# Kernel optimization log

Hardware: AMD Instinct MI355X
Metric: run time of the kernel (lower is better)

Reference implementation:

```python
import jax, jax.numpy as jnp
import numpy as np

B, T, C, H = 2, 2048, 1024, 16
HD = C // H  # head dim = 64


def setup_inputs() -> dict:
    key = jax.random.key(0)
    k1, k2, k3 = jax.random.split(key, 3)
    scale = 0.02
    x = jax.random.normal(k1, (B, T, C), dtype=jnp.float32)
    w_attn = jax.random.normal(k2, (C, 3 * C), dtype=jnp.float32) * scale
    b_attn = jnp.zeros((3 * C,), dtype=jnp.float32)
    w_proj = jax.random.normal(k3, (C, C), dtype=jnp.float32) * scale
    b_proj = jnp.zeros((C,), dtype=jnp.float32)
    return {"x": x, "w_attn": w_attn, "b_attn": b_attn, "w_proj": w_proj, "b_proj": b_proj}


def reference(x, w_attn, b_attn, w_proj, b_proj):
    b, t, c = x.shape
    qkv = x @ w_attn + b_attn  # [B,T,3C]
    q, k, v = jnp.split(qkv, 3, axis=-1)
    # [B,T,C] -> [B,H,T,HD]
    q = q.reshape(b, t, H, HD).transpose(0, 2, 1, 3)
    k = k.reshape(b, t, H, HD).transpose(0, 2, 1, 3)
    v = v.reshape(b, t, H, HD).transpose(0, 2, 1, 3)
    att = jnp.einsum('bhqd,bhkd->bhqk', q, k) * (1.0 / jnp.sqrt(jnp.float32(HD)))
    causal = jnp.tril(jnp.ones((t, t), dtype=bool))  # [T,T]
    att = jnp.where(causal[None, None, :, :], att, jnp.float32(-jnp.inf))
    att = jax.nn.softmax(att, axis=-1)
    y = jnp.einsum('bhqk,bhkd->bhqd', att, v)
    y = y.transpose(0, 2, 1, 3).reshape(b, t, c)
    return y @ w_proj + b_proj
```

## Files before the change

kernel.cpp:

```cpp
#include <hip/hip_runtime.h>


typedef unsigned short u16;
typedef unsigned short u16x8 __attribute__((ext_vector_type(8)));
typedef __bf16 bf16x8 __attribute__((ext_vector_type(8)));
typedef __bf16 bf16x4 __attribute__((ext_vector_type(4)));
typedef float f32x4 __attribute__((ext_vector_type(4)));

#define MFMA16(a, b, c) __builtin_amdgcn_mfma_f32_16x16x32_bf16(a, b, c, 0, 0, 0)

static __device__ __forceinline__ u16 f2b(float f) {
  union { float f; unsigned int i; } x; x.f = f;
  unsigned int r = x.i + 0x7fffu + ((x.i >> 16) & 1u);
  return (u16)(r >> 16);
}
static __device__ __forceinline__ float b2f(u16 u) {
  union { unsigned int i; float f; } x; x.i = ((unsigned int)u) << 16; return x.f;
}

static __device__ __forceinline__ void gload_lds16(const u16* g, u16* l) {
#if defined(__HIP_DEVICE_COMPILE__)
  __builtin_amdgcn_global_load_lds(
      (const __attribute__((address_space(1))) unsigned int*)g,
      (__attribute__((address_space(3))) unsigned int*)l,
      16, 0, 0);
#else
  (void)g; (void)l;
#endif
}

__global__ __launch_bounds__(256) void cast_f32_bf16(
    const float* __restrict__ in, u16* __restrict__ out) {
  int i = (blockIdx.x * 256 + threadIdx.x) * 8;
  float4 a = *(const float4*)&in[i];
  float4 b = *(const float4*)&in[i + 4];
  u16x8 o;
  o[0] = f2b(a.x); o[1] = f2b(a.y); o[2] = f2b(a.z); o[3] = f2b(a.w);
  o[4] = f2b(b.x); o[5] = f2b(b.y); o[6] = f2b(b.z); o[7] = f2b(b.w);
  *(u16x8*)&out[i] = o;
}

__global__ __launch_bounds__(256) void transpose_f32_bf16(
    const float* __restrict__ in, u16* __restrict__ out, int R, int Cc) {
  __shared__ u16 tile[32][33];
  int bx = blockIdx.x, by = blockIdx.y;
  int tx = threadIdx.x, ty = threadIdx.y;
#pragma unroll
  for (int i = 0; i < 4; i++) {
    int r = by * 32 + ty + i * 8;
    int c = bx * 32 + tx;
    tile[ty + i * 8][tx] = f2b(in[r * Cc + c]);
  }
  __syncthreads();
#pragma unroll
  for (int i = 0; i < 4; i++) {
    int r = bx * 32 + ty + i * 8;
    int c = by * 32 + tx;
    out[r * R + c] = tile[tx][ty + i * 8];
  }
}

__global__ __launch_bounds__(256) void transpose_v(
    const u16* __restrict__ in, u16* __restrict__ out) {
  int bh = blockIdx.y;
  int t = blockIdx.x * 128 + (threadIdx.x & 127);
  int dg = (threadIdx.x >> 7) * 32;
  const u16* src = in + (bh * 2048 + t) * 64;
  u16* dst = out + bh * 64 * 2048 + t;
#pragma unroll
  for (int i = 0; i < 32; i++) {
    int d = dg + i;
    dst[d * 2048] = src[d];
  }
}

template <int MODE>
__global__ __launch_bounds__(256, 2) void gemm_bt(
    const u16* __restrict__ A, const u16* __restrict__ Bt,
    const float* __restrict__ bias, float* __restrict__ out,
    u16* __restrict__ Qb, u16* __restrict__ Kb, u16* __restrict__ Vb,
    int M, int N, int K) {
  __shared__ u16 lA[128 * 32];
  __shared__ u16 lB[128 * 32];

  const int tid = threadIdx.x;
  const int lane = tid & 63;
  const int w = tid >> 6;
  const int wm = (w >> 1) * 64, wn = (w & 1) * 64;
  const int l15 = lane & 15, quad = lane >> 4;
  const int m0 = blockIdx.y * 128, n0 = blockIdx.x * 128;

  const int srow = lane >> 2;
  const int scol = (lane & 3) * 8;

  f32x4 acc[4][4] = {};

  for (int k0 = 0; k0 < K; k0 += 32) {
    __syncthreads();
#pragma unroll
    for (int h = 0; h < 2; h++) {
      int r = h * 64 + w * 16 + srow;
      gload_lds16(&A[(m0 + r) * K + k0 + scol], &lA[h * 2048 + w * 512 + lane * 8]);
      gload_lds16(&Bt[(n0 + r) * K + k0 + scol], &lB[h * 2048 + w * 512 + lane * 8]);
    }
    __syncthreads();

    bf16x8 af[4], bfr[4];
#pragma unroll
    for (int mi = 0; mi < 4; mi++)
      af[mi] = *(const bf16x8*)&lA[(wm + mi * 16 + l15) * 32 + quad * 8];
#pragma unroll
    for (int ni = 0; ni < 4; ni++)
      bfr[ni] = *(const bf16x8*)&lB[(wn + ni * 16 + l15) * 32 + quad * 8];
#pragma unroll
    for (int mi = 0; mi < 4; mi++)
#pragma unroll
      for (int ni = 0; ni < 4; ni++)
        acc[mi][ni] = MFMA16(af[mi], bfr[ni], acc[mi][ni]);
  }

#pragma unroll
  for (int mi = 0; mi < 4; mi++) {
#pragma unroll
    for (int ni = 0; ni < 4; ni++) {
      int n = n0 + wn + ni * 16 + l15;
      float bv = bias[n];
#pragma unroll
      for (int reg = 0; reg < 4; reg++) {
        int m = m0 + wm + mi * 16 + quad * 4 + reg;
        float v = acc[mi][ni][reg] + bv;
        if (MODE == 1) {
          out[m * N + n] = v;
        } else {
          int which = n >> 10;
          if (which == 1) v *= 0.18033688011112042f;
          int hn = n & 1023;
          int hh = hn >> 6, d = hn & 63;
          int b = m >> 11, t = m & 2047;
          u16* dst = (which == 0) ? Qb : ((which == 1) ? Kb : Vb);
          dst[(((b << 4) + hh) * 2048 + t) * 64 + d] = f2b(v);
        }
      }
    }
  }
}

__global__ __launch_bounds__(256, 4) void attn_split(
    const u16* __restrict__ Qg, const u16* __restrict__ Kg,
    const u16* __restrict__ Vt, u16* __restrict__ Yg,
    u16* __restrict__ Opart, float* __restrict__ lpart) {
  __shared__ u16 lk[64 * 72];
  __shared__ u16 lvt[64 * 72];

  const int x = blockIdx.x;
  const int bh = blockIdx.y;
  int qt, s, ns;
  if (x < 8)       { qt = x;                s = 0;            ns = 1; }
  else if (x < 24) { int r = x - 8;  qt = 8  + (r >> 1); s = r & 1; ns = 2; }
  else if (x < 48) { int r = x - 24; qt = 16 + r / 3;    s = r % 3; ns = 3; }
  else             { int r = x - 48; qt = 24 + (r >> 2); s = r & 3; ns = 4; }
  const int kts = s * 8;
  const int kend = (kts + 8 < qt + 1) ? (kts + 8) : (qt + 1);

  const int tid = threadIdx.x;
  const int lane = tid & 63;
  const int w = tid >> 6;
  const int l15 = lane & 15, quad = lane >> 4;
  const int qbase = qt * 64;
  const int base = bh * 2048 * 64;
  const int vbase = bh * 64 * 2048;

  const int sr = tid >> 3;
  const int sc = (tid & 7) * 8;

  const u16* qrow = Qg + base + (qbase + w * 16 + l15) * 64;
  bf16x8 bq0 = *(const bf16x8*)&qrow[quad * 8];
  bf16x8 bq1 = *(const bf16x8*)&qrow[32 + quad * 8];

  u16x8 onesu = {0x3F80, 0x3F80, 0x3F80, 0x3F80, 0x3F80, 0x3F80, 0x3F80, 0x3F80};
  bf16x8 ones = *(const bf16x8*)&onesu;

  const u16* kp = Kg + base;
  const u16* vp = Vt + vbase;

  u16x8 kr[2], vr[2];
  {
    int kvb = kts * 64;
#pragma unroll
    for (int h = 0; h < 2; h++) {
      int r = sr + h * 32;
      kr[h] = *(const u16x8*)&kp[(kvb + r) * 64 + sc];
      vr[h] = *(const u16x8*)&vp[r * 2048 + kvb + sc];
    }
  }

  f32x4 oacc[4] = {};
  f32x4 lacc = {};

  for (int kt = kts; kt < kend; kt++) {
    __syncthreads();
#pragma unroll
    for (int h = 0; h < 2; h++) {
      int r = sr + h * 32;
      *(u16x8*)&lk[r * 72 + sc] = kr[h];
      *(u16x8*)&lvt[r * 72 + sc] = vr[h];
    }
    __syncthreads();
    if (kt + 1 < kend) {
      int kvb = (kt + 1) * 64;
#pragma unroll
      for (int h = 0; h < 2; h++) {
        int r = sr + h * 32;
        kr[h] = *(const u16x8*)&kp[(kvb + r) * 64 + sc];
        vr[h] = *(const u16x8*)&vp[r * 2048 + kvb + sc];
      }
    }

    const bool diag = (kt == qt);
    const int qloc = w * 16 + l15;

#pragma unroll
    for (int u = 0; u < 2; u++) {
      bf16x8 pa;
#pragma unroll
      for (int half = 0; half < 2; half++) {
        int nt = 2 * u + half;
        bf16x8 ak0 = *(const bf16x8*)&lk[(nt * 16 + l15) * 72 + quad * 8];
        bf16x8 ak1 = *(const bf16x8*)&lk[(nt * 16 + l15) * 72 + 32 + quad * 8];
        f32x4 st = {};
        st = MFMA16(ak0, bq0, st);
        st = MFMA16(ak1, bq1, st);
#pragma unroll
        for (int reg = 0; reg < 4; reg++) {
          float sv = st[reg];
          if (diag && (nt * 16 + quad * 4 + reg) > qloc) sv = -1e30f;
          pa[half * 4 + reg] = (__bf16)exp2f(sv);
        }
      }
      lacc = MFMA16(pa, ones, lacc);
#pragma unroll
      for (int dt = 0; dt < 4; dt++) {
        const u16* vrow = &lvt[(dt * 16 + l15) * 72 + u * 32 + quad * 4];
        bf16x4 lo = *(const bf16x4*)&vrow[0];
        bf16x4 hi = *(const bf16x4*)&vrow[16];
        bf16x8 bv;
#pragma unroll
        for (int j = 0; j < 4; j++) { bv[j] = lo[j]; bv[4 + j] = hi[j]; }
        oacc[dt] = MFMA16(pa, bv, oacc[dt]);
      }
    }
  }

  if (ns == 1) {
    const int b = bh >> 4, hh = bh & 15;
    float inv[4];
#pragma unroll
    for (int reg = 0; reg < 4; reg++) inv[reg] = 1.0f / lacc[reg];
#pragma unroll
    for (int dt = 0; dt < 4; dt++)
#pragma unroll
      for (int reg = 0; reg < 4; reg++) {
        int q = qbase + w * 16 + quad * 4 + reg;
        int col = hh * 64 + dt * 16 + l15;
        Yg[(b * 2048 + q) * 1024 + col] = f2b(oacc[dt][reg] * inv[reg]);
      }
  } else {
    const int p = bh * 80 + x;
    u16* op = Opart + p * 4096 + (w * 16) * 64;
#pragma unroll
    for (int dt = 0; dt < 4; dt++)
#pragma unroll
      for (int reg = 0; reg < 4; reg++)
        op[(quad * 4 + reg) * 64 + dt * 16 + l15] = f2b(oacc[dt][reg]);
    if (l15 == 0) {
#pragma unroll
      for (int reg = 0; reg < 4; reg++)
        lpart[p * 64 + w * 16 + quad * 4 + reg] = lacc[reg];
    }
  }
}

__global__ __launch_bounds__(256) void attn_combine(
    const u16* __restrict__ Opart, const float* __restrict__ lpart,
    u16* __restrict__ Yg) {
  const int qt = 8 + blockIdx.x;
  const int bh = blockIdx.y;
  const int tid = threadIdx.x;
  const int row = tid >> 2;
  const int cg = (tid & 3) * 16;
  int xb, ns;
  if (qt < 16)      { xb = 8  + (qt - 8) * 2;  ns = 2; }
  else if (qt < 24) { xb = 24 + (qt - 16) * 3; ns = 3; }
  else              { xb = 48 + (qt - 24) * 4; ns = 4; }

  float acc[16] = {};
  float lsum = 0.f;
  for (int i = 0; i < ns; i++) {
    int p = bh * 80 + xb + i;
    lsum += lpart[p * 64 + row];
    const u16* oprow = Opart + p * 4096 + row * 64 + cg;
    u16x8 a = *(const u16x8*)&oprow[0];
    u16x8 b = *(const u16x8*)&oprow[8];
#pragma unroll
    for (int j = 0; j < 8; j++) { acc[j] += b2f(a[j]); acc[8 + j] += b2f(b[j]); }
  }
  float inv = 1.0f / lsum;
  u16x8 o0, o1;
#pragma unroll
  for (int j = 0; j < 8; j++) { o0[j] = f2b(acc[j] * inv); o1[j] = f2b(acc[8 + j] * inv); }
  const int b = bh >> 4, hh = bh & 15;
  u16* y = Yg + ((long)(b * 2048 + qt * 64 + row)) * 1024 + hh * 64 + cg;
  *(u16x8*)&y[0] = o0;
  *(u16x8*)&y[8] = o1;
}

__global__ __launch_bounds__(256, 4) void attn_kernel(
    const u16* __restrict__ Qg, const u16* __restrict__ Kg,
    const u16* __restrict__ Vt, u16* __restrict__ Yg) {
  __shared__ u16 lk[64 * 72];
  __shared__ u16 lvt[64 * 72];

  const int qt = 31 - blockIdx.x;
  const int bh = blockIdx.y;
  const int tid = threadIdx.x;
  const int lane = tid & 63;
  const int w = tid >> 6;
  const int l15 = lane & 15, quad = lane >> 4;
  const int qbase = qt * 64;
  const int base = bh * 2048 * 64;
  const int vbase = bh * 64 * 2048;
  const int sr = tid >> 3;
  const int sc = (tid & 7) * 8;

  const u16* qrow = Qg + base + (qbase + w * 16 + l15) * 64;
  bf16x8 bq0 = *(const bf16x8*)&qrow[quad * 8];
  bf16x8 bq1 = *(const bf16x8*)&qrow[32 + quad * 8];

  u16x8 onesu = {0x3F80, 0x3F80, 0x3F80, 0x3F80, 0x3F80, 0x3F80, 0x3F80, 0x3F80};
  bf16x8 ones = *(const bf16x8*)&onesu;

  const u16* kp = Kg + base;
  const u16* vp = Vt + vbase;

  u16x8 kr[2], vr[2];
#pragma unroll
  for (int h = 0; h < 2; h++) {
    int r = sr + h * 32;
    kr[h] = *(const u16x8*)&kp[r * 64 + sc];
    vr[h] = *(const u16x8*)&vp[r * 2048 + sc];
  }

  f32x4 oacc[4] = {};
  f32x4 lacc = {};

  for (int kt = 0; kt <= qt; kt++) {
    __syncthreads();
#pragma unroll
    for (int h = 0; h < 2; h++) {
      int r = sr + h * 32;
      *(u16x8*)&lk[r * 72 + sc] = kr[h];
      *(u16x8*)&lvt[r * 72 + sc] = vr[h];
    }
    __syncthreads();
    if (kt < qt) {
      int kvb = (kt + 1) * 64;
#pragma unroll
      for (int h = 0; h < 2; h++) {
        int r = sr + h * 32;
        kr[h] = *(const u16x8*)&kp[(kvb + r) * 64 + sc];
        vr[h] = *(const u16x8*)&vp[r * 2048 + kvb + sc];
      }
    }

    const bool diag = (kt == qt);
    const int qloc = w * 16 + l15;
#pragma unroll
    for (int u = 0; u < 2; u++) {
      bf16x8 pa;
#pragma unroll
      for (int half = 0; half < 2; half++) {
        int nt = 2 * u + half;
        bf16x8 ak0 = *(const bf16x8*)&lk[(nt * 16 + l15) * 72 + quad * 8];
        bf16x8 ak1 = *(const bf16x8*)&lk[(nt * 16 + l15) * 72 + 32 + quad * 8];
        f32x4 st = {};
        st = MFMA16(ak0, bq0, st);
        st = MFMA16(ak1, bq1, st);
#pragma unroll
        for (int reg = 0; reg < 4; reg++) {
          float sv = st[reg];
          if (diag && (nt * 16 + quad * 4 + reg) > qloc) sv = -1e30f;
          pa[half * 4 + reg] = (__bf16)exp2f(sv);
        }
      }
      lacc = MFMA16(pa, ones, lacc);
#pragma unroll
      for (int dt = 0; dt < 4; dt++) {
        const u16* vrow = &lvt[(dt * 16 + l15) * 72 + u * 32 + quad * 4];
        bf16x4 lo = *(const bf16x4*)&vrow[0];
        bf16x4 hi = *(const bf16x4*)&vrow[16];
        bf16x8 bv;
#pragma unroll
        for (int j = 0; j < 4; j++) { bv[j] = lo[j]; bv[4 + j] = hi[j]; }
        oacc[dt] = MFMA16(pa, bv, oacc[dt]);
      }
    }
  }

  const int b = bh >> 4, hh = bh & 15;
  float inv[4];
#pragma unroll
  for (int reg = 0; reg < 4; reg++) inv[reg] = 1.0f / lacc[reg];
#pragma unroll
  for (int dt = 0; dt < 4; dt++)
#pragma unroll
    for (int reg = 0; reg < 4; reg++) {
      int q = qbase + w * 16 + quad * 4 + reg;
      int col = hh * 64 + dt * 16 + l15;
      Yg[(b * 2048 + q) * 1024 + col] = f2b(oacc[dt][reg] * inv[reg]);
    }
}

extern "C" void kernel_launch(void* const* d_in, const int* in_sizes, int n_in,
                              void* d_out, int out_size, void* d_ws, size_t ws_size,
                              hipStream_t stream) {
  const float* x      = (const float*)d_in[0];
  const float* w_attn = (const float*)d_in[1];
  const float* b_attn = (const float*)d_in[2];
  const float* w_proj = (const float*)d_in[3];
  const float* b_proj = (const float*)d_in[4];
  float* out = (float*)d_out;

  char* ws = (char*)d_ws;
  u16* wattnT = (u16*)(ws);
  u16* wprojT = (u16*)(ws + 6291456);
  u16* xb     = (u16*)(ws + 8388608);
  u16* Vt     = xb;
  u16* Qb     = (u16*)(ws + 16777216);
  u16* Kb     = (u16*)(ws + 25165824);
  u16* Vb     = (u16*)(ws + 33554432);
  u16* Yb     = (u16*)(ws + 41943040);
  u16* Opart  = (u16*)(ws + 50331648);
  float* lpart = (float*)(ws + 71303168);

  const bool split = (ws_size >= 71958528ULL);

  cast_f32_bf16<<<2048, 256, 0, stream>>>(x, xb);
  transpose_f32_bf16<<<dim3(96, 32), dim3(32, 8), 0, stream>>>(w_attn, wattnT, 1024, 3072);
  transpose_f32_bf16<<<dim3(32, 32), dim3(32, 8), 0, stream>>>(w_proj, wprojT, 1024, 1024);
  gemm_bt<0><<<dim3(24, 32), 256, 0, stream>>>(xb, wattnT, b_attn, nullptr,
                                               Qb, Kb, Vb, 4096, 3072, 1024);
  transpose_v<<<dim3(16, 32), 256, 0, stream>>>(Vb, Vt);
  if (split) {
    attn_split<<<dim3(80, 32), 256, 0, stream>>>(Qb, Kb, Vt, Yb, Opart, lpart);
    attn_combine<<<dim3(24, 32), 256, 0, stream>>>(Opart, lpart, Yb);
  } else {
    attn_kernel<<<dim3(32, 32), 256, 0, stream>>>(Qb, Kb, Vt, Yb);
  }
  gemm_bt<1><<<dim3(8, 32), 256, 0, stream>>>(Yb, wprojT, b_proj, out,
                                              nullptr, nullptr, nullptr, 4096, 1024, 1024);
}
```

Before: 200.3 us.

## Process two query tiles per attention block to reuse K/V tiles

Each split-attention block now handles a pair of adjacent 64-row query tiles (128 rows), computing two score/probability streams against each loaded K/V tile. This halves the K/V global loads and LDS staging per query row and halves the grid size. The blocks are also launched in reverse order so the heaviest work starts first. In exchange, register pressure rises from doubling the accumulators, and there are fewer, larger blocks, which may lower occupancy. The combine kernel and the partial buffer layout are adjusted to match.

```diff
diff --git a/kernel.cpp b/kernel.cpp
--- a/kernel.cpp
+++ b/kernel.cpp
@@ -152,30 +152,36 @@
   __shared__ u16 lk[64 * 72];
   __shared__ u16 lvt[64 * 72];
 
-  const int x = blockIdx.x;
+  const int x = 39 - blockIdx.x;
   const int bh = blockIdx.y;
-  int qt, s, ns;
-  if (x < 8)       { qt = x;                s = 0;            ns = 1; }
-  else if (x < 24) { int r = x - 8;  qt = 8  + (r >> 1); s = r & 1; ns = 2; }
-  else if (x < 48) { int r = x - 24; qt = 16 + r / 3;    s = r % 3; ns = 3; }
-  else             { int r = x - 48; qt = 24 + (r >> 2); s = r & 3; ns = 4; }
+  int p, s, ns;
+  if (x < 4)       { p = x;          s = 0;           ns = 1; }
+  else if (x < 12) { int r = x - 4;  p = 4 + (r >> 1);  s = r & 1;  ns = 2; }
+  else if (x < 24) { int r = x - 12; p = 8 + r / 3;     s = r % 3;  ns = 3; }
+  else             { int r = x - 24; p = 12 + (r >> 2); s = r & 3;  ns = 4; }
   const int kts = s * 8;
-  const int kend = (kts + 8 < qt + 1) ? (kts + 8) : (qt + 1);
+  const int ktotal = 2 * p + 2;
+  const int kend = (kts + 8 < ktotal) ? (kts + 8) : ktotal;
+  const int qtA = 2 * p;
 
   const int tid = threadIdx.x;
   const int lane = tid & 63;
   const int w = tid >> 6;
   const int l15 = lane & 15, quad = lane >> 4;
-  const int qbase = qt * 64;
   const int base = bh * 2048 * 64;
   const int vbase = bh * 64 * 2048;
 
   const int sr = tid >> 3;
   const int sc = (tid & 7) * 8;
 
-  const u16* qrow = Qg + base + (qbase + w * 16 + l15) * 64;
-  bf16x8 bq0 = *(const bf16x8*)&qrow[quad * 8];
-  bf16x8 bq1 = *(const bf16x8*)&qrow[32 + quad * 8];
+  const u16* qrA = Qg + base + (qtA * 64 + w * 16 + l15) * 64;
+  bf16x8 bq0A = *(const bf16x8*)&qrA[quad * 8];
+  bf16x8 bq1A = *(const bf16x8*)&qrA[32 + quad * 8];
+  const u16* qrB = qrA + 64 * 64;
+  bf16x8 bq0B = *(const bf16x8*)&qrB[quad * 8];
+  bf16x8 bq1B = *(const bf16x8*)&qrB[32 + quad * 8];
+
+  const int qgA = qtA * 64 + w * 16 + l15;
 
   u16x8 onesu = {0x3F80, 0x3F80, 0x3F80, 0x3F80, 0x3F80, 0x3F80, 0x3F80, 0x3F80};
   bf16x8 ones = *(const bf16x8*)&onesu;
@@ -194,8 +200,8 @@
     }
   }
 
-  f32x4 oacc[4] = {};
-  f32x4 lacc = {};
+  f32x4 oA[4] = {}, oB[4] = {};
+  f32x4 lA4 = {}, lB4 = {};
 
   for (int kt = kts; kt < kend; kt++) {
     __syncthreads();
@@ -216,28 +222,37 @@
       }
     }
 
-    const bool diag = (kt == qt);
-    const int qloc = w * 16 + l15;
+    const bool mA = (kt >= qtA);
+    const bool mB = (kt == qtA + 1);
 
 #pragma unroll
     for (int u = 0; u < 2; u++) {
-      bf16x8 pa;
+      bf16x8 paA, paB;
 #pragma unroll
       for (int half = 0; half < 2; half++) {
         int nt = 2 * u + half;
         bf16x8 ak0 = *(const bf16x8*)&lk[(nt * 16 + l15) * 72 + quad * 8];
         bf16x8 ak1 = *(const bf16x8*)&lk[(nt * 16 + l15) * 72 + 32 + quad * 8];
-        f32x4 st = {};
-        st = MFMA16(ak0, bq0, st);
-        st = MFMA16(ak1, bq1, st);
+        f32x4 stA = {};
+        stA = MFMA16(ak0, bq0A, stA);
+        stA = MFMA16(ak1, bq1A, stA);
+        f32x4 stB = {};
+        stB = MFMA16(ak0, bq0B, stB);
+        stB = MFMA16(ak1, bq1B, stB);
+        int kv0 = kt * 64 + nt * 16 + quad * 4;
 #pragma unroll
         for (int reg = 0; reg < 4; reg++) {
-          float sv = st[reg];
-          if (diag && (nt * 16 + quad * 4 + reg) > qloc) sv = -1e30f;
-          pa[half * 4 + reg] = (__bf16)exp2f(sv);
+          int kv = kv0 + reg;
+          float svA = stA[reg];
+          if (mA && kv > qgA) svA = -1e30f;
+          float svB = stB[reg];
+          if (mB && kv > qgA + 64) svB = -1e30f;
+          paA[half * 4 + reg] = (__bf16)exp2f(svA);
+          paB[half * 4 + reg] = (__bf16)exp2f(svB);
         }
       }
-      lacc = MFMA16(pa, ones, lacc);
+      lA4 = MFMA16(paA, ones, lA4);
+      lB4 = MFMA16(paB, ones, lB4);
 #pragma unroll
       for (int dt = 0; dt < 4; dt++) {
         const u16* vrow = &lvt[(dt * 16 + l15) * 72 + u * 32 + quad * 4];
@@ -246,36 +261,47 @@
         bf16x8 bv;
 #pragma unroll
         for (int j = 0; j < 4; j++) { bv[j] = lo[j]; bv[4 + j] = hi[j]; }
-        oacc[dt] = MFMA16(pa, bv, oacc[dt]);
+        oA[dt] = MFMA16(paA, bv, oA[dt]);
+        oB[dt] = MFMA16(paB, bv, oB[dt]);
       }
     }
   }
 
   if (ns == 1) {
     const int b = bh >> 4, hh = bh & 15;
-    float inv[4];
-#pragma unroll
-    for (int reg = 0; reg < 4; reg++) inv[reg] = 1.0f / lacc[reg];
+    float invA[4], invB[4];
+#pragma unroll
+    for (int reg = 0; reg < 4; reg++) {
+      invA[reg] = 1.0f / lA4[reg];
+      invB[reg] = 1.0f / lB4[reg];
+    }
 #pragma unroll
     for (int dt = 0; dt < 4; dt++)
 #pragma unroll
       for (int reg = 0; reg < 4; reg++) {
-        int q = qbase + w * 16 + quad * 4 + reg;
+        int qA = qtA * 64 + w * 16 + quad * 4 + reg;
         int col = hh * 64 + dt * 16 + l15;
-        Yg[(b * 2048 + q) * 1024 + col] = f2b(oacc[dt][reg] * inv[reg]);
+        Yg[(b * 2048 + qA) * 1024 + col] = f2b(oA[dt][reg] * invA[reg]);
+        Yg[(b * 2048 + qA + 64) * 1024 + col] = f2b(oB[dt][reg] * invB[reg]);
       }
   } else {
-    const int p = bh * 80 + x;
-    u16* op = Opart + p * 4096 + (w * 16) * 64;
+    const int pidx = bh * 40 + x;
+    u16* op = Opart + pidx * 8192;
 #pragma unroll
     for (int dt = 0; dt < 4; dt++)
 #pragma unroll
-      for (int reg = 0; reg < 4; reg++)
-        op[(quad * 4 + reg) * 64 + dt * 16 + l15] = f2b(oacc[dt][reg]);
+      for (int reg = 0; reg < 4; reg++) {
+        int rA = w * 16 + quad * 4 + reg;
+        op[rA * 64 + dt * 16 + l15] = f2b(oA[dt][reg]);
+        op[(rA + 64) * 64 + dt * 16 + l15] = f2b(oB[dt][reg]);
+      }
     if (l15 == 0) {
 #pragma unroll
-      for (int reg = 0; reg < 4; reg++)
-        lpart[p * 64 + w * 16 + quad * 4 + reg] = lacc[reg];
+      for (int reg = 0; reg < 4; reg++) {
+        int rA = w * 16 + quad * 4 + reg;
+        lpart[pidx * 128 + rA] = lA4[reg];
+        lpart[pidx * 128 + rA + 64] = lB4[reg];
+      }
     }
   }
 }
@@ -283,35 +309,39 @@
 __global__ __launch_bounds__(256) void attn_combine(
     const u16* __restrict__ Opart, const float* __restrict__ lpart,
     u16* __restrict__ Yg) {
-  const int qt = 8 + blockIdx.x;
+  const int pp = 4 + blockIdx.x;
   const int bh = blockIdx.y;
   const int tid = threadIdx.x;
-  const int row = tid >> 2;
-  const int cg = (tid & 3) * 16;
+  const int row = tid >> 1;
+  const int cg = (tid & 1) * 32;
   int xb, ns;
-  if (qt < 16)      { xb = 8  + (qt - 8) * 2;  ns = 2; }
-  else if (qt < 24) { xb = 24 + (qt - 16) * 3; ns = 3; }
-  else              { xb = 48 + (qt - 24) * 4; ns = 4; }
-
-  float acc[16] = {};
+  if (pp < 8)       { xb = 4  + (pp - 4) * 2;  ns = 2; }
+  else if (pp < 12) { xb = 12 + (pp - 8) * 3;  ns = 3; }
+  else              { xb = 24 + (pp - 12) * 4; ns = 4; }
+
+  float acc[32] = {};
   float lsum = 0.f;
   for (int i = 0; i < ns; i++) {
-    int p = bh * 80 + xb + i;
-    lsum += lpart[p * 64 + row];
-    const u16* oprow = Opart + p * 4096 + row * 64 + cg;
-    u16x8 a = *(const u16x8*)&oprow[0];
-    u16x8 b = *(const u16x8*)&oprow[8];
-#pragma unroll
-    for (int j = 0; j < 8; j++) { acc[j] += b2f(a[j]); acc[8 + j] += b2f(b[j]); }
+    int pidx = bh * 40 + xb + i;
+    lsum += lpart[pidx * 128 + row];
+    const u16* oprow = Opart + pidx * 8192 + row * 64 + cg;
+#pragma unroll
+    for (int v = 0; v < 4; v++) {
+      u16x8 a = *(const u16x8*)&oprow[v * 8];
+#pragma unroll
+      for (int j = 0; j < 8; j++) acc[v * 8 + j] += b2f(a[j]);
+    }
   }
   float inv = 1.0f / lsum;
-  u16x8 o0, o1;
-#pragma unroll
-  for (int j = 0; j < 8; j++) { o0[j] = f2b(acc[j] * inv); o1[j] = f2b(acc[8 + j] * inv); }
   const int b = bh >> 4, hh = bh & 15;
-  u16* y = Yg + ((long)(b * 2048 + qt * 64 + row)) * 1024 + hh * 64 + cg;
-  *(u16x8*)&y[0] = o0;
-  *(u16x8*)&y[8] = o1;
+  u16* y = Yg + ((long)(b * 2048 + pp * 128 + row)) * 1024 + hh * 64 + cg;
+#pragma unroll
+  for (int v = 0; v < 4; v++) {
+    u16x8 o;
+#pragma unroll
+    for (int j = 0; j < 8; j++) o[j] = f2b(acc[v * 8 + j] * inv);
+    *(u16x8*)&y[v * 8] = o;
+  }
 }
 
 __global__ __launch_bounds__(256, 4) void attn_kernel(
@@ -451,8 +481,8 @@
                                                Qb, Kb, Vb, 4096, 3072, 1024);
   transpose_v<<<dim3(16, 32), 256, 0, stream>>>(Vb, Vt);
   if (split) {
-    attn_split<<<dim3(80, 32), 256, 0, stream>>>(Qb, Kb, Vt, Yb, Opart, lpart);
-    attn_combine<<<dim3(24, 32), 256, 0, stream>>>(Opart, lpart, Yb);
+    attn_split<<<dim3(40, 32), 256, 0, stream>>>(Qb, Kb, Vt, Yb, Opart, lpart);
+    attn_combine<<<dim3(12, 32), 256, 0, stream>>>(Opart, lpart, Yb);
   } else {
     attn_kernel<<<dim3(32, 32), 256, 0, stream>>>(Qb, Kb, Vt, Yb);
   }
```

After: 201.1 us. No clear change (+0.4%).
